# Performance work log

Measured on AMD Instinct MI355X. Metric: run time of the kernel, lower is better.

## Reference

```python
import jax, jax.numpy as jnp
import numpy as np

WINDOW_SIZE = 11
SIGMA = 1.5


def _gaussian_window(window_size, sigma, channel, dtype):
    xs = np.arange(window_size, dtype=np.float64)
    g = np.exp(-((xs - window_size // 2) ** 2) / (2.0 * sigma ** 2))
    g = (g / g.sum()).astype(np.float32)
    w2d = np.outer(g, g)  # [K, K]
    # depthwise kernel: [channel, 1, K, K] (OIHW with feature_group_count=channel)
    w = np.broadcast_to(w2d[None, None], (channel, 1, window_size, window_size))
    return jnp.asarray(np.ascontiguousarray(w), dtype=dtype)


def _depthwise_conv(img, window, channel):
    pad = WINDOW_SIZE // 2
    return jax.lax.conv_general_dilated(
        img, window,
        window_strides=(1, 1),
        padding=((pad, pad), (pad, pad)),
        dimension_numbers=("NCHW", "OIHW", "NCHW"),
        feature_group_count=channel,
    )


def setup_inputs() -> dict:
    key = jax.random.key(0)
    k1, k2 = jax.random.split(key)
    x = jax.random.uniform(k1, (16, 3, 512, 512), dtype=jnp.float32)
    y = jax.random.uniform(k2, (16, 3, 512, 512), dtype=jnp.float32)
    return {"x": x, "y": y}


def reference(x, y):
    channel = x.shape[1]
    window = _gaussian_window(WINDOW_SIZE, SIGMA, channel, x.dtype)

    mu_x = _depthwise_conv(x, window, channel)
    mu_y = _depthwise_conv(y, window, channel)
    mu_x_sq = mu_x * mu_x
    mu_y_sq = mu_y * mu_y
    mu_xy = mu_x * mu_y

    sigma_x = _depthwise_conv(x * x, window, channel) - mu_x_sq
    sigma_y = _depthwise_conv(y * y, window, channel) - mu_y_sq
    sigma_xy = _depthwise_conv(x * y, window, channel) - mu_xy

    C1 = 0.01 ** 2
    C2 = 0.03 ** 2
    ssim_n = (2.0 * mu_xy + C1) * (2.0 * sigma_xy + C2)
    ssim_d = (mu_x_sq + mu_y_sq + C1) * (sigma_x + sigma_y + C2)
    ssim_map = ssim_n / (ssim_d + 1e-08)
    # size_average=True
    return jnp.mean(ssim_map)
```

## Files before the change

kernel.cpp:

```cpp
#include <hip/hip_runtime.h>
#include <cmath>

constexpr int IMG_H = 512;
constexpr int IMG_W = 512;
constexpr int PLANES = 48;
constexpr int R_OUT = 8;
constexpr int BANDS = IMG_H / R_OUT;
constexpr int PSTR = 512;
constexpr int NSLOT = 64;
constexpr int NBLK = PLANES * BANDS;
constexpr long long TOTAL_PIX = (long long)PLANES * IMG_H * IMG_W;

struct GWin { float g[11]; };

__device__ __forceinline__ int swzd(int d) { return d ^ (((d >> 5) & 7) << 2); }
__device__ __forceinline__ int swzd4(int b) { return b ^ ((b >> 3) & 7); }

template<bool CHK>
__device__ __forceinline__ float2 ld2(const float* __restrict__ base, int gr, int c0) {
    if (CHK && (unsigned)gr >= (unsigned)IMG_H) return make_float2(0.f, 0.f);
    return *(const float2*)(base + (size_t)gr * IMG_W + c0);
}

__device__ __forceinline__ float hpass8(const float* __restrict__ fr0,
                                        int l, const int (&pb)[6],
                                        const GWin& win) {
    float m[5][8];
#pragma unroll
    for (int f = 0; f < 5; ++f) {
        const float* fr = fr0 + f * PSTR;
        float w24[24];
#pragma unroll
        for (int B = 0; B < 6; ++B) {
            const float4 v = *(const float4*)&fr[pb[B]];
            w24[4 * B + 0] = v.x;  w24[4 * B + 1] = v.y;
            w24[4 * B + 2] = v.z;  w24[4 * B + 3] = v.w;
        }
        if (l == 0)  { w24[3] = w24[4] = w24[5] = w24[6] = w24[7] = 0.f; }
        if (l == 63) { w24[16] = w24[17] = w24[18] = w24[19] = w24[20] = 0.f; }
#pragma unroll
        for (int j = 0; j < 8; ++j) {
            float s = 0.f;
#pragma unroll
            for (int k = 0; k < 11; ++k) s += win.g[k] * w24[j + 3 + k];
            m[f][j] = s;
        }
    }
    float ls = 0.f;
#pragma unroll
    for (int u = 0; u < 8; ++u) {
        const float mx  = m[0][u], my  = m[1][u];
        const float mxx = m[2][u], myy = m[3][u], mxy = m[4][u];
        const float mu_x_sq = mx * mx;
        const float mu_y_sq = my * my;
        const float mu_xy   = mx * my;
        const float sig_x  = mxx - mu_x_sq;
        const float sig_y  = myy - mu_y_sq;
        const float sig_xy = mxy - mu_xy;
        const float C1 = 0.01f * 0.01f;
        const float C2 = 0.03f * 0.03f;
        const float n = (2.f * mu_xy + C1) * (2.f * sig_xy + C2);
        const float d = (mu_x_sq + mu_y_sq + C1) * (sig_x + sig_y + C2);
        ls += n * __builtin_amdgcn_rcpf(d + 1e-8f);
    }
    return ls;
}

template<int I0>
__device__ __forceinline__ void vconv4(const float2 (&xr)[18], const float2 (&yr)[18],
                                       float* __restrict__ hb, int pws,
                                       const GWin& win) {
    float2 acc[4][5];
#pragma unroll
    for (int j = 0; j < 4; ++j)
#pragma unroll
        for (int f = 0; f < 5; ++f) acc[j][f] = make_float2(0.f, 0.f);
#pragma unroll
    for (int k = 0; k < 14; ++k) {
        const float2 xv = xr[I0 + k], yv = yr[I0 + k];
        const float2 pxx = make_float2(xv.x * xv.x, xv.y * xv.y);
        const float2 pyy = make_float2(yv.x * yv.x, yv.y * yv.y);
        const float2 pxy = make_float2(xv.x * yv.x, xv.y * yv.y);
#pragma unroll
        for (int j = 0; j < 4; ++j) {
            const int t = k - j;
            if (t >= 0 && t <= 10) {
                const float g = win.g[t];
                acc[j][0].x += g * xv.x;   acc[j][0].y += g * xv.y;
                acc[j][1].x += g * yv.x;   acc[j][1].y += g * yv.y;
                acc[j][2].x += g * pxx.x;  acc[j][2].y += g * pxx.y;
                acc[j][3].x += g * pyy.x;  acc[j][3].y += g * pyy.y;
                acc[j][4].x += g * pxy.x;  acc[j][4].y += g * pxy.y;
            }
        }
    }
#pragma unroll
    for (int j = 0; j < 4; ++j)
#pragma unroll
        for (int f = 0; f < 5; ++f)
            *(float2*)&hb[(j * 5 + f) * PSTR + pws] = acc[j][f];
}

template<bool CHK>
__device__ __forceinline__ float band_body(const float* __restrict__ xp,
                                           const float* __restrict__ yp,
                                           int r0, int c0, int tid,
                                           float* __restrict__ hb,
                                           const GWin& win)
{
    const int pws = swzd(2 * tid);
    const int row = tid >> 6, l = tid & 63;
    int pb[6];
#pragma unroll
    for (int B = 0; B < 6; ++B) {
        int blk = 2 * l - 2 + B;
        blk = blk < 0 ? 0 : (blk > 127 ? 127 : blk);
        pb[B] = 4 * swzd4(blk);
    }

    float2 xr[18], yr[18];
#pragma unroll
    for (int i = 0; i < 14; ++i) {
        xr[i] = ld2<CHK>(xp, r0 - 5 + i, c0);
        yr[i] = ld2<CHK>(yp, r0 - 5 + i, c0);
    }

    vconv4<0>(xr, yr, hb, pws, win);
    __syncthreads();

#pragma unroll
    for (int i = 14; i < 18; ++i) {
        xr[i] = ld2<CHK>(xp, r0 - 5 + i, c0);
        yr[i] = ld2<CHK>(yp, r0 - 5 + i, c0);
    }

    float lsum = hpass8(hb + row * 5 * PSTR, l, pb, win);
    __syncthreads();

    vconv4<4>(xr, yr, hb, pws, win);
    __syncthreads();

    lsum += hpass8(hb + row * 5 * PSTR, l, pb, win);
    return lsum;
}

__global__ __launch_bounds__(256)
void ssim_share_kernel(const float* __restrict__ x,
                       const float* __restrict__ y,
                       double* __restrict__ accum,
                       GWin win)
{
    __shared__ __align__(16) float hbuf[4 * 5 * PSTR];

    const int tid = threadIdx.x;
    const int bid = blockIdx.x;
    const int L   = (bid & 7) * (NBLK / 8) + (bid >> 3);
    const int band  = L & (BANDS - 1);
    const int plane = L >> 6;
    const int r0    = band * R_OUT;
    const int c0    = tid * 2;

    const float* __restrict__ xp = x + (size_t)plane * (IMG_H * IMG_W);
    const float* __restrict__ yp = y + (size_t)plane * (IMG_H * IMG_W);

    float lsum;
    if (band >= 1 && band <= BANDS - 2)
        lsum = band_body<false>(xp, yp, r0, c0, tid, hbuf, win);
    else
        lsum = band_body<true>(xp, yp, r0, c0, tid, hbuf, win);

#pragma unroll
    for (int off = 32; off; off >>= 1) lsum += __shfl_down(lsum, off);
    if ((tid & 63) == 0) {
        const int wid = L * 4 + (tid >> 6);
        atomicAdd(&accum[(wid & (NSLOT - 1)) * 8], (double)lsum);
    }
}

__global__ void ssim_finalize_kernel(const double* __restrict__ accum,
                                     float* __restrict__ out)
{
    double s = 0.0;
    for (int i = 0; i < NSLOT; ++i) s += accum[i * 8];
    out[0] = (float)(s / (double)TOTAL_PIX);
}

extern "C" void kernel_launch(void* const* d_in, const int* in_sizes, int n_in,
                              void* d_out, int out_size, void* d_ws, size_t ws_size,
                              hipStream_t stream) {
    const float* x = (const float*)d_in[0];
    const float* y = (const float*)d_in[1];
    float* out = (float*)d_out;
    double* accum = (double*)d_ws;

    GWin win;
    {
        double g[11], s = 0.0;
        for (int i = 0; i < 11; ++i) {
            double d = (double)i - 5.0;
            g[i] = std::exp(-(d * d) / (2.0 * 1.5 * 1.5));
            s += g[i];
        }
        for (int i = 0; i < 11; ++i) win.g[i] = (float)(g[i] / s);
    }

    (void)hipMemsetAsync(d_ws, 0, NSLOT * 8 * sizeof(double), stream);

    ssim_share_kernel<<<NBLK, 256, 0, stream>>>(x, y, accum, win);
    ssim_finalize_kernel<<<1, 1, 0, stream>>>(accum, out);
}
```

Measured before the change: 69.43 us.

## Process band two rows at a time with rolling register window

```diff
diff --git a/kernel.cpp b/kernel.cpp
--- a/kernel.cpp
+++ b/kernel.cpp
@@ -22,33 +22,35 @@
     return *(const float2*)(base + (size_t)gr * IMG_W + c0);
 }
 
-__device__ __forceinline__ float hpass8(const float* __restrict__ fr0,
-                                        int l, const int (&pb)[6],
+__device__ __forceinline__ float hpass4(const float* __restrict__ fr0,
+                                        int l, const int (&pb)[5],
                                         const GWin& win) {
-    float m[5][8];
+    float m[5][4];
 #pragma unroll
     for (int f = 0; f < 5; ++f) {
         const float* fr = fr0 + f * PSTR;
-        float w24[24];
-#pragma unroll
-        for (int B = 0; B < 6; ++B) {
+        float w20[20];
+#pragma unroll
+        for (int B = 0; B < 5; ++B) {
             const float4 v = *(const float4*)&fr[pb[B]];
-            w24[4 * B + 0] = v.x;  w24[4 * B + 1] = v.y;
-            w24[4 * B + 2] = v.z;  w24[4 * B + 3] = v.w;
-        }
-        if (l == 0)  { w24[3] = w24[4] = w24[5] = w24[6] = w24[7] = 0.f; }
-        if (l == 63) { w24[16] = w24[17] = w24[18] = w24[19] = w24[20] = 0.f; }
-#pragma unroll
-        for (int j = 0; j < 8; ++j) {
+            w20[4 * B + 0] = v.x;  w20[4 * B + 1] = v.y;
+            w20[4 * B + 2] = v.z;  w20[4 * B + 3] = v.w;
+        }
+        if (l == 0)   { w20[3] = w20[4] = w20[5] = w20[6] = w20[7] = 0.f; }
+        if (l == 1)   { w20[3] = 0.f; }
+        if (l == 126) { w20[16] = 0.f; }
+        if (l == 127) { w20[12] = w20[13] = w20[14] = w20[15] = w20[16] = 0.f; }
+#pragma unroll
+        for (int j = 0; j < 4; ++j) {
             float s = 0.f;
 #pragma unroll
-            for (int k = 0; k < 11; ++k) s += win.g[k] * w24[j + 3 + k];
+            for (int k = 0; k < 11; ++k) s += win.g[k] * w20[j + 3 + k];
             m[f][j] = s;
         }
     }
     float ls = 0.f;
 #pragma unroll
-    for (int u = 0; u < 8; ++u) {
+    for (int u = 0; u < 4; ++u) {
         const float mx  = m[0][u], my  = m[1][u];
         const float mxx = m[2][u], myy = m[3][u], mxy = m[4][u];
         const float mu_x_sq = mx * mx;
@@ -66,41 +68,6 @@
     return ls;
 }
 
-template<int I0>
-__device__ __forceinline__ void vconv4(const float2 (&xr)[18], const float2 (&yr)[18],
-                                       float* __restrict__ hb, int pws,
-                                       const GWin& win) {
-    float2 acc[4][5];
-#pragma unroll
-    for (int j = 0; j < 4; ++j)
-#pragma unroll
-        for (int f = 0; f < 5; ++f) acc[j][f] = make_float2(0.f, 0.f);
-#pragma unroll
-    for (int k = 0; k < 14; ++k) {
-        const float2 xv = xr[I0 + k], yv = yr[I0 + k];
-        const float2 pxx = make_float2(xv.x * xv.x, xv.y * xv.y);
-        const float2 pyy = make_float2(yv.x * yv.x, yv.y * yv.y);
-        const float2 pxy = make_float2(xv.x * yv.x, xv.y * yv.y);
-#pragma unroll
-        for (int j = 0; j < 4; ++j) {
-            const int t = k - j;
-            if (t >= 0 && t <= 10) {
-                const float g = win.g[t];
-                acc[j][0].x += g * xv.x;   acc[j][0].y += g * xv.y;
-                acc[j][1].x += g * yv.x;   acc[j][1].y += g * yv.y;
-                acc[j][2].x += g * pxx.x;  acc[j][2].y += g * pxx.y;
-                acc[j][3].x += g * pyy.x;  acc[j][3].y += g * pyy.y;
-                acc[j][4].x += g * pxy.x;  acc[j][4].y += g * pxy.y;
-            }
-        }
-    }
-#pragma unroll
-    for (int j = 0; j < 4; ++j)
-#pragma unroll
-        for (int f = 0; f < 5; ++f)
-            *(float2*)&hb[(j * 5 + f) * PSTR + pws] = acc[j][f];
-}
-
 template<bool CHK>
 __device__ __forceinline__ float band_body(const float* __restrict__ xp,
                                            const float* __restrict__ yp,
@@ -109,48 +76,91 @@
                                            const GWin& win)
 {
     const int pws = swzd(2 * tid);
-    const int row = tid >> 6, l = tid & 63;
-    int pb[6];
-#pragma unroll
-    for (int B = 0; B < 6; ++B) {
-        int blk = 2 * l - 2 + B;
+    const int row = tid >> 7, l = tid & 127;
+    int pb[5];
+#pragma unroll
+    for (int B = 0; B < 5; ++B) {
+        int blk = l - 2 + B;
         blk = blk < 0 ? 0 : (blk > 127 ? 127 : blk);
         pb[B] = 4 * swzd4(blk);
     }
 
-    float2 xr[18], yr[18];
-#pragma unroll
-    for (int i = 0; i < 14; ++i) {
+    float2 xr[12], yr[12];
+#pragma unroll
+    for (int i = 0; i < 12; ++i) {
         xr[i] = ld2<CHK>(xp, r0 - 5 + i, c0);
         yr[i] = ld2<CHK>(yp, r0 - 5 + i, c0);
     }
 
-    vconv4<0>(xr, yr, hb, pws, win);
-    __syncthreads();
-
-#pragma unroll
-    for (int i = 14; i < 18; ++i) {
-        xr[i] = ld2<CHK>(xp, r0 - 5 + i, c0);
-        yr[i] = ld2<CHK>(yp, r0 - 5 + i, c0);
-    }
-
-    float lsum = hpass8(hb + row * 5 * PSTR, l, pb, win);
-    __syncthreads();
-
-    vconv4<4>(xr, yr, hb, pws, win);
-    __syncthreads();
-
-    lsum += hpass8(hb + row * 5 * PSTR, l, pb, win);
+    float lsum = 0.f;
+
+#pragma unroll 1
+    for (int rr = 0; rr < 4; ++rr) {
+        const int rbase = r0 + 2 * rr;
+
+        float2 acc[2][5];
+#pragma unroll
+        for (int j = 0; j < 2; ++j)
+#pragma unroll
+            for (int f = 0; f < 5; ++f) acc[j][f] = make_float2(0.f, 0.f);
+
+#pragma unroll
+        for (int k = 0; k < 12; ++k) {
+            const float2 xv = xr[k], yv = yr[k];
+            const float2 pxx = make_float2(xv.x * xv.x, xv.y * xv.y);
+            const float2 pyy = make_float2(yv.x * yv.x, yv.y * yv.y);
+            const float2 pxy = make_float2(xv.x * yv.x, xv.y * yv.y);
+            if (k < 11) {
+                const float g = win.g[k];
+                acc[0][0].x += g * xv.x;   acc[0][0].y += g * xv.y;
+                acc[0][1].x += g * yv.x;   acc[0][1].y += g * yv.y;
+                acc[0][2].x += g * pxx.x;  acc[0][2].y += g * pxx.y;
+                acc[0][3].x += g * pyy.x;  acc[0][3].y += g * pyy.y;
+                acc[0][4].x += g * pxy.x;  acc[0][4].y += g * pxy.y;
+            }
+            if (k > 0) {
+                const float g = win.g[k - 1];
+                acc[1][0].x += g * xv.x;   acc[1][0].y += g * xv.y;
+                acc[1][1].x += g * yv.x;   acc[1][1].y += g * yv.y;
+                acc[1][2].x += g * pxx.x;  acc[1][2].y += g * pxx.y;
+                acc[1][3].x += g * pyy.x;  acc[1][3].y += g * pyy.y;
+                acc[1][4].x += g * pxy.x;  acc[1][4].y += g * pxy.y;
+            }
+        }
+
+#pragma unroll
+        for (int j = 0; j < 2; ++j)
+#pragma unroll
+            for (int f = 0; f < 5; ++f)
+                *(float2*)&hb[(j * 5 + f) * PSTR + pws] = acc[j][f];
+
+        __syncthreads();
+
+        float2 px0{}, py0{}, px1{}, py1{};
+        if (rr < 3) {
+            px0 = ld2<CHK>(xp, rbase + 7, c0);  py0 = ld2<CHK>(yp, rbase + 7, c0);
+            px1 = ld2<CHK>(xp, rbase + 8, c0);  py1 = ld2<CHK>(yp, rbase + 8, c0);
+        }
+
+        lsum += hpass4(hb + row * 5 * PSTR, l, pb, win);
+
+        __syncthreads();
+
+#pragma unroll
+        for (int k = 0; k < 10; ++k) { xr[k] = xr[k + 2]; yr[k] = yr[k + 2]; }
+        xr[10] = px0;  yr[10] = py0;
+        xr[11] = px1;  yr[11] = py1;
+    }
     return lsum;
 }
 
 __global__ __launch_bounds__(256)
-void ssim_share_kernel(const float* __restrict__ x,
-                       const float* __restrict__ y,
-                       double* __restrict__ accum,
-                       GWin win)
+void ssim_r18_kernel(const float* __restrict__ x,
+                     const float* __restrict__ y,
+                     double* __restrict__ accum,
+                     GWin win)
 {
-    __shared__ __align__(16) float hbuf[4 * 5 * PSTR];
+    __shared__ __align__(16) float hbuf[2 * 5 * PSTR];
 
     const int tid = threadIdx.x;
     const int bid = blockIdx.x;
@@ -206,6 +216,6 @@
 
     (void)hipMemsetAsync(d_ws, 0, NSLOT * 8 * sizeof(double), stream);
 
-    ssim_share_kernel<<<NBLK, 256, 0, stream>>>(x, y, accum, win);
+    ssim_r18_kernel<<<NBLK, 256, 0, stream>>>(x, y, accum, win);
     ssim_finalize_kernel<<<1, 1, 0, stream>>>(accum, out);
 }
```

Result: slower. 77.80 us (+12.1%).

## Reformulate SSIM with sum/difference fields to need four convolutions instead of five

Applied to the files above, without the earlier changes.

```diff
diff --git a/kernel.cpp b/kernel.cpp
--- a/kernel.cpp
+++ b/kernel.cpp
@@ -25,9 +25,9 @@
 __device__ __forceinline__ float hpass8(const float* __restrict__ fr0,
                                         int l, const int (&pb)[6],
                                         const GWin& win) {
-    float m[5][8];
-#pragma unroll
-    for (int f = 0; f < 5; ++f) {
+    float m[4][8];
+#pragma unroll
+    for (int f = 0; f < 4; ++f) {
         const float* fr = fr0 + f * PSTR;
         float w24[24];
 #pragma unroll
@@ -49,19 +49,19 @@
     float ls = 0.f;
 #pragma unroll
     for (int u = 0; u < 8; ++u) {
-        const float mx  = m[0][u], my  = m[1][u];
-        const float mxx = m[2][u], myy = m[3][u], mxy = m[4][u];
-        const float mu_x_sq = mx * mx;
-        const float mu_y_sq = my * my;
-        const float mu_xy   = mx * my;
-        const float sig_x  = mxx - mu_x_sq;
-        const float sig_y  = myy - mu_y_sq;
-        const float sig_xy = mxy - mu_xy;
+        const float sb  = m[0][u];
+        const float db  = m[1][u];
+        const float css = m[2][u];
+        const float cdd = m[3][u];
+        const float A = sb * sb;
+        const float B = db * db;
         const float C1 = 0.01f * 0.01f;
         const float C2 = 0.03f * 0.03f;
-        const float n = (2.f * mu_xy + C1) * (2.f * sig_xy + C2);
-        const float d = (mu_x_sq + mu_y_sq + C1) * (sig_x + sig_y + C2);
-        ls += n * __builtin_amdgcn_rcpf(d + 1e-8f);
+        const float n1 = 0.5f * (A - B) + C1;
+        const float n2 = 0.5f * ((css - cdd) - (A - B)) + C2;
+        const float d1 = 0.5f * (A + B) + C1;
+        const float d2 = 0.5f * ((css + cdd) - (A + B)) + C2;
+        ls += (n1 * n2) * __builtin_amdgcn_rcpf(d1 * d2 + 1e-8f);
     }
     return ls;
 }
@@ -70,35 +70,35 @@
 __device__ __forceinline__ void vconv4(const float2 (&xr)[18], const float2 (&yr)[18],
                                        float* __restrict__ hb, int pws,
                                        const GWin& win) {
-    float2 acc[4][5];
+    float2 acc[4][4];
 #pragma unroll
     for (int j = 0; j < 4; ++j)
 #pragma unroll
-        for (int f = 0; f < 5; ++f) acc[j][f] = make_float2(0.f, 0.f);
+        for (int f = 0; f < 4; ++f) acc[j][f] = make_float2(0.f, 0.f);
 #pragma unroll
     for (int k = 0; k < 14; ++k) {
         const float2 xv = xr[I0 + k], yv = yr[I0 + k];
-        const float2 pxx = make_float2(xv.x * xv.x, xv.y * xv.y);
-        const float2 pyy = make_float2(yv.x * yv.x, yv.y * yv.y);
-        const float2 pxy = make_float2(xv.x * yv.x, xv.y * yv.y);
+        const float2 sv = make_float2(xv.x + yv.x, xv.y + yv.y);
+        const float2 dv = make_float2(xv.x - yv.x, xv.y - yv.y);
+        const float2 ssv = make_float2(sv.x * sv.x, sv.y * sv.y);
+        const float2 ddv = make_float2(dv.x * dv.x, dv.y * dv.y);
 #pragma unroll
         for (int j = 0; j < 4; ++j) {
             const int t = k - j;
             if (t >= 0 && t <= 10) {
                 const float g = win.g[t];
-                acc[j][0].x += g * xv.x;   acc[j][0].y += g * xv.y;
-                acc[j][1].x += g * yv.x;   acc[j][1].y += g * yv.y;
-                acc[j][2].x += g * pxx.x;  acc[j][2].y += g * pxx.y;
-                acc[j][3].x += g * pyy.x;  acc[j][3].y += g * pyy.y;
-                acc[j][4].x += g * pxy.x;  acc[j][4].y += g * pxy.y;
+                acc[j][0].x += g * sv.x;   acc[j][0].y += g * sv.y;
+                acc[j][1].x += g * dv.x;   acc[j][1].y += g * dv.y;
+                acc[j][2].x += g * ssv.x;  acc[j][2].y += g * ssv.y;
+                acc[j][3].x += g * ddv.x;  acc[j][3].y += g * ddv.y;
             }
         }
     }
 #pragma unroll
     for (int j = 0; j < 4; ++j)
 #pragma unroll
-        for (int f = 0; f < 5; ++f)
-            *(float2*)&hb[(j * 5 + f) * PSTR + pws] = acc[j][f];
+        for (int f = 0; f < 4; ++f)
+            *(float2*)&hb[(j * 4 + f) * PSTR + pws] = acc[j][f];
 }
 
 template<bool CHK>
@@ -134,23 +134,23 @@
         yr[i] = ld2<CHK>(yp, r0 - 5 + i, c0);
     }
 
-    float lsum = hpass8(hb + row * 5 * PSTR, l, pb, win);
+    float lsum = hpass8(hb + row * 4 * PSTR, l, pb, win);
     __syncthreads();
 
     vconv4<4>(xr, yr, hb, pws, win);
     __syncthreads();
 
-    lsum += hpass8(hb + row * 5 * PSTR, l, pb, win);
+    lsum += hpass8(hb + row * 4 * PSTR, l, pb, win);
     return lsum;
 }
 
 __global__ __launch_bounds__(256)
-void ssim_share_kernel(const float* __restrict__ x,
-                       const float* __restrict__ y,
-                       double* __restrict__ accum,
-                       GWin win)
+void ssim_sd_kernel(const float* __restrict__ x,
+                    const float* __restrict__ y,
+                    double* __restrict__ accum,
+                    GWin win)
 {
-    __shared__ __align__(16) float hbuf[4 * 5 * PSTR];
+    __shared__ __align__(16) float hbuf[4 * 4 * PSTR];
 
     const int tid = threadIdx.x;
     const int bid = blockIdx.x;
@@ -206,6 +206,6 @@
 
     (void)hipMemsetAsync(d_ws, 0, NSLOT * 8 * sizeof(double), stream);
 
-    ssim_share_kernel<<<NBLK, 256, 0, stream>>>(x, y, accum, win);
+    ssim_sd_kernel<<<NBLK, 256, 0, stream>>>(x, y, accum, win);
     ssim_finalize_kernel<<<1, 1, 0, stream>>>(accum, out);
 }
```

After: 63.20 us. 1.1x faster.
